# Kernel optimization log

Measured on AMD Instinct MI355X. Metric: run time of the kernel, lower is better.

The kernel has to match this reference:

```python
import jax, jax.numpy as jnp
import numpy as np

N_NODES = 100000
D = 128
ATT = 128
P_EDGE_TYPES = 3
N_EDGES = 1600000
BATCH = 65536


def gcn_conv(x, W, b, src, dst, n):
    # PyG GCNConv: add self loops, symmetric D^{-1/2} (A+I) D^{-1/2} x W + b
    h = x @ W                                   # [N, D]
    ones = jnp.ones(src.shape[0], x.dtype)
    deg = jax.ops.segment_sum(ones, dst, num_segments=n) + 1.0  # +1 self loop
    dinv = jax.lax.rsqrt(deg)
    norm = dinv[src] * dinv[dst]                # [E]
    out = jax.ops.segment_sum(h[src] * norm[:, None], dst, num_segments=n)
    out = out + h * (dinv * dinv)[:, None]      # self-loop message, norm = dinv_i^2
    return out + b


def semantic_attention(z, P, W, b, q):
    # z: [P*N, D] -> per-edge-type scalar attention, softmax over P, weighted sum
    att = jnp.tanh(z @ W + b) @ q               # [P*N]
    att = att.reshape(P, -1).mean(axis=1)       # [P]
    att = jax.nn.softmax(att)
    zp = z.reshape(P, -1, z.shape[-1])          # [P, N, D]
    return jnp.einsum('p,pnd->nd', att, zp)     # [N, D]


def gnn_branch(x0, edge_index, W1, b1, W2, b2, n):
    outs = []
    for t in range(edge_index.shape[0]):        # fixed small set of edge types
        src, dst = edge_index[t, 0], edge_index[t, 1]
        h = jax.nn.relu(gcn_conv(x0, W1, b1, src, dst, n))
        h = jax.nn.relu(gcn_conv(h, W2, b2, src, dst, n))
        outs.append(h)
    return jnp.concatenate(outs, axis=0)        # [P*N, D]


def setup_inputs() -> dict:
    key = jax.random.key(0)
    ks = jax.random.split(key, 16)
    x = jax.random.normal(ks[0], (N_NODES, D), jnp.float32)
    edge_index = jax.random.randint(ks[1], (P_EDGE_TYPES, 2, N_EDGES), 0, N_NODES, jnp.int64)
    perm = jax.random.permutation(ks[2], N_NODES).astype(jnp.int64)
    summary_vetor = jax.random.normal(ks[3], (D,), jnp.float32)
    s = 1.0 / np.sqrt(D)
    params = dict(
        W_lin=jax.random.normal(ks[4], (D, D), jnp.float32) * s,
        b_lin=jnp.zeros((D,), jnp.float32),
        W1=jax.random.normal(ks[5], (D, D), jnp.float32) * s,
        b1=jnp.zeros((D,), jnp.float32),
        W2=jax.random.normal(ks[6], (D, D), jnp.float32) * s,
        b2=jnp.zeros((D,), jnp.float32),
        W_sem=jax.random.normal(ks[7], (D, ATT), jnp.float32) * s,
        b_sem=jnp.zeros((ATT,), jnp.float32),
        q_sem=jax.random.normal(ks[8], (ATT,), jnp.float32) * (1.0 / np.sqrt(ATT)),
        W_disc=jax.random.normal(ks[9], (D, D), jnp.float32) * s,
        b_disc=jnp.zeros((), jnp.float32),
    )
    return dict(x=x, edge_index=edge_index, perm=perm,
                summary_vetor=summary_vetor, Batch_size=BATCH, **params)


def reference(x, edge_index, perm, summary_vetor, Batch_size,
              W_lin, b_lin, W1, b1, W2, b2, W_sem, b_sem, q_sem, W_disc, b_disc):
    n = x.shape[0]
    x_pos = jax.nn.relu(x @ W_lin + b_lin)
    x_neg = jax.nn.relu(x[perm] @ W_lin + b_lin)

    z_pos = gnn_branch(x_pos, edge_index, W1, b1, W2, b2, n)
    z_neg = gnn_branch(x_neg, edge_index, W1, b1, W2, b2, n)

    P = edge_index.shape[0]
    att_pos = semantic_attention(z_pos, P, W_sem, b_sem, q_sem)[:Batch_size]
    att_neg = semantic_attention(z_neg, P, W_sem, b_sem, q_sem)[:Batch_size]

    summary_in = att_pos.mean(axis=0)           # AvgReadout
    summary = 0.5 * (summary_vetor + summary_in)

    # Discriminator: bilinear score against broadcast summary
    c = W_disc @ summary                        # [D]
    sc_pos = att_pos @ c + b_disc               # [B]
    sc_neg = att_neg @ c + b_disc               # [B]
    ret = jnp.concatenate([sc_pos, sc_neg], axis=0)  # [2B]
    return ret, summary
```

## Files before the change

kernel.cpp:

```cpp
#include <hip/hip_runtime.h>

#define D_ 128
#define BATCH_ 65536
#define BSH 10
#define TILE_ 16384

typedef _Float16 f16;
typedef _Float16 h2v __attribute__((ext_vector_type(2)));
typedef _Float16 f16x8 __attribute__((ext_vector_type(8)));
typedef float f32x4 __attribute__((ext_vector_type(4)));

__global__ void k_zero32(uint32_t* p, long long n) {
    long long i = (long long)blockIdx.x * blockDim.x + threadIdx.x;
    long long st = (long long)gridDim.x * blockDim.x;
    for (; i < n; i += st) p[i] = 0u;
}

__global__ void k_sentinel(float* p, long long n) {
    long long i = (long long)blockIdx.x * blockDim.x + threadIdx.x;
    long long st = (long long)gridDim.x * blockDim.x;
    for (; i < n; i += st) p[i] = -12345.0f;
}

__global__ void k_wt(const float* __restrict__ W, f16* __restrict__ Wt) {
    int t = blockIdx.x * 256 + threadIdx.x;
    int k = t >> 7, c = t & 127;
    Wt[c * 128 + k] = (f16)W[k * 128 + c];
}

__global__ void k_gath(const uint32_t* __restrict__ src, const int* __restrict__ perm,
                       uint32_t* __restrict__ dst, int N) {
    int i = blockIdx.x * 256 + threadIdx.x;
    if (i >= N * 64) return;
    int row = i >> 6, col = i & 63;
    dst[i] = src[((size_t)perm[row] << 6) + col];
}

__global__ void k_hist(const int* __restrict__ ei, int* __restrict__ bcnt,
                       int E, int nbt, int nbuk) {
    __shared__ int hist[512];
    for (int i = threadIdx.x; i < 512; i += 256) hist[i] = 0;
    __syncthreads();
    long long tot = 3LL * E;
    long long i = (long long)blockIdx.x * 256 + threadIdx.x;
    long long st = (long long)gridDim.x * 256;
    for (; i < tot; i += st) {
        int t = (i >= E) + (i >= 2LL * E);
        long long w = i - (long long)t * E;
        int dst = ei[(long long)t * 2 * E + E + w];
        atomicAdd(&hist[t * nbt + (dst >> BSH)], 1);
    }
    __syncthreads();
    for (int i2 = threadIdx.x; i2 < nbuk; i2 += 256)
        if (hist[i2]) atomicAdd(&bcnt[i2], hist[i2]);
}

__global__ void k_bscan(const int* __restrict__ bcnt, int* __restrict__ bbase,
                        int* __restrict__ bcur, int nbuk) {
    __shared__ int s[512];
    int t = threadIdx.x;
    int v = (t < nbuk) ? bcnt[t] : 0;
    s[t] = v;
    __syncthreads();
    for (int off = 1; off < 512; off <<= 1) {
        int a = (t >= off) ? s[t - off] : 0;
        __syncthreads();
        s[t] += a;
        __syncthreads();
    }
    if (t < nbuk) {
        int e = s[t] - v;
        bbase[t] = e;
        bcur[t] = e;
        if (t == nbuk - 1) bbase[nbuk] = s[t];
    }
}

__global__ __launch_bounds__(256) void k_scatter(const int* __restrict__ ei,
                                                 int* __restrict__ bcur,
                                                 uint32_t* __restrict__ pairs,
                                                 int E, int nbt, int nbuk) {
    __shared__ int hist[512];
    __shared__ int base[512];
    long long tot = 3LL * E;
    long long w0 = (long long)blockIdx.x * TILE_;
    long long w1 = w0 + TILE_ < tot ? w0 + TILE_ : tot;
    for (int i = threadIdx.x; i < 512; i += 256) hist[i] = 0;
    __syncthreads();
    for (long long e = w0 + threadIdx.x; e < w1; e += 256) {
        int t = (e >= E) + (e >= 2LL * E);
        long long w = e - (long long)t * E;
        int dst = ei[(long long)t * 2 * E + E + w];
        atomicAdd(&hist[t * nbt + (dst >> BSH)], 1);
    }
    __syncthreads();
    for (int i = threadIdx.x; i < nbuk; i += 256) {
        int c = hist[i];
        base[i] = c ? atomicAdd(&bcur[i], c) : 0;
        hist[i] = 0;
    }
    __syncthreads();
    for (long long e = w0 + threadIdx.x; e < w1; e += 256) {
        int t = (e >= E) + (e >= 2LL * E);
        long long w = e - (long long)t * E;
        int src = ei[(long long)t * 2 * E + w];
        int dst = ei[(long long)t * 2 * E + E + w];
        int b = t * nbt + (dst >> BSH);
        int off = atomicAdd(&hist[b], 1);
        pairs[base[b] + off] = (uint32_t)src | ((uint32_t)(dst & ((1 << BSH) - 1)) << 22);
    }
}

__global__ __launch_bounds__(256) void k_bucket(const uint32_t* __restrict__ pairs,
                                                const int* __restrict__ bbase,
                                                int* __restrict__ rowstart,
                                                float* __restrict__ dinv,
                                                int* __restrict__ csr,
                                                int N, int nbt, int nbuk, int L) {
    __shared__ int cnt[1024];
    __shared__ int pref[1024];
    __shared__ int sums[256];
    int b = blockIdx.x;
    int t = b / nbt, bb = b - t * nbt;
    int dst0 = bb << BSH;
    int ndst = (N - dst0 < 1024) ? (N - dst0) : 1024;
    int e0 = bbase[b], e1 = bbase[b + 1];
    int tid = threadIdx.x;
    for (int i = tid; i < 1024; i += 256) cnt[i] = 0;
    __syncthreads();
    for (int e = e0 + tid; e < e1; e += 256) atomicAdd(&cnt[pairs[e] >> 22], 1);
    __syncthreads();
    int i0 = tid * 4;
    int c0 = cnt[i0], c1 = cnt[i0 + 1], c2 = cnt[i0 + 2], c3 = cnt[i0 + 3];
    int s4 = c0 + c1 + c2 + c3;
    sums[tid] = s4;
    __syncthreads();
    for (int off = 1; off < 256; off <<= 1) {
        int v = (tid >= off) ? sums[tid - off] : 0;
        __syncthreads();
        sums[tid] += v;
        __syncthreads();
    }
    int run = sums[tid] - s4;
    pref[i0] = run; run += c0;
    pref[i0 + 1] = run; run += c1;
    pref[i0 + 2] = run; run += c2;
    pref[i0 + 3] = run;
    __syncthreads();
    for (int d = tid; d < ndst; d += 256) {
        int r = t * N + dst0 + d;
        rowstart[r] = e0 + pref[d];
        dinv[r] = rsqrtf((float)cnt[d] + 1.0f);
    }
    if (b == nbuk - 1 && tid == 0) rowstart[L] = e1;
    __syncthreads();
    for (int e = e0 + tid; e < e1; e += 256) {
        uint32_t u = pairs[e];
        int d = u >> 22;
        int pos = e0 + atomicAdd(&pref[d], 1);
        csr[pos] = (int)(u & ((1u << 22) - 1));
    }
}

__global__ void k_wedge(const int* __restrict__ csr, const float* __restrict__ dinv,
                        f16* __restrict__ w16, int N, int E) {
    long long tot = 3LL * E;
    long long i = (long long)blockIdx.x * 256 + threadIdx.x;
    long long st = (long long)gridDim.x * 256;
    for (; i < tot; i += st) {
        int t = (i >= E) + (i >= 2LL * E);
        w16[i] = (f16)dinv[t * N + csr[i]];
    }
}

__global__ __launch_bounds__(256) void k_mgemm(const void* __restrict__ in, int in_f32,
                                               const f16* __restrict__ Wt,
                                               const float* __restrict__ bias,
                                               f16* __restrict__ outh, int n, int relu) {
    int l = threadIdx.x & 63, wid = threadIdx.x >> 6;
    int row0 = blockIdx.x * 128 + wid * 32;
    int r = l & 15, kg = l >> 4;
    f32x4 acc[2][8] = {};
#pragma unroll
    for (int kk = 0; kk < 4; kk++) {
        int off = kk * 32 + kg * 8;
        f16x8 a[2];
#pragma unroll
        for (int h = 0; h < 2; h++) {
            int arow = row0 + h * 16 + r;
            f16x8 av = {};
            if (arow < n) {
                if (in_f32) {
                    const float* inf = (const float*)in + (size_t)arow * D_ + off;
                    float4 v0 = *(const float4*)inf;
                    float4 v1 = *(const float4*)(inf + 4);
                    av[0] = (f16)v0.x; av[1] = (f16)v0.y; av[2] = (f16)v0.z; av[3] = (f16)v0.w;
                    av[4] = (f16)v1.x; av[5] = (f16)v1.y; av[6] = (f16)v1.z; av[7] = (f16)v1.w;
                } else {
                    av = *(const f16x8*)((const f16*)in + (size_t)arow * D_ + off);
                }
            }
            a[h] = av;
        }
#pragma unroll
        for (int ct = 0; ct < 8; ct++) {
            f16x8 b = *(const f16x8*)(Wt + (size_t)(ct * 16 + r) * D_ + off);
            acc[0][ct] = __builtin_amdgcn_mfma_f32_16x16x32_f16(a[0], b, acc[0][ct], 0, 0, 0);
            acc[1][ct] = __builtin_amdgcn_mfma_f32_16x16x32_f16(a[1], b, acc[1][ct], 0, 0, 0);
        }
    }
#pragma unroll
    for (int h = 0; h < 2; h++) {
#pragma unroll
        for (int ct = 0; ct < 8; ct++) {
            int c = ct * 16 + r;
            float bs = bias ? bias[c] : 0.0f;
#pragma unroll
            for (int j = 0; j < 4; j++) {
                int rr = row0 + h * 16 + kg * 4 + j;
                if (rr >= n) continue;
                float o = acc[h][ct][j] + bs;
                if (relu) o = fmaxf(o, 0.0f);
                outh[(size_t)rr * D_ + c] = (f16)o;
            }
        }
    }
}

__global__ __launch_bounds__(256) void k_spmm1g(const f16* __restrict__ gsrc,
                                                const int* __restrict__ csr,
                                                const f16* __restrict__ w16,
                                                const int* __restrict__ rowstart,
                                                const float* __restrict__ dinv,
                                                const float* __restrict__ bias,
                                                const f16* __restrict__ Wt,
                                                f16* __restrict__ outG,
                                                int N, int rows, int src_typed) {
    __shared__ f16 hs[16][136];
    int tid = (int)threadIdx.x;
    int lp = tid & 15;
    int row16 = tid >> 4;
    int gw0 = blockIdx.x * 16;
    int gw = gw0 + row16;
    bool valid = gw < rows;
    float a[8] = {};
    if (valid) {
        int t = (gw >= N) + (gw >= 2 * N);
        int tbase = t * N;
        int sbase = src_typed ? tbase : 0;
        int self = src_typed ? gw : gw - tbase;
        int s0 = rowstart[gw], s1 = rowstart[gw + 1];
        float di = dinv[gw];
        size_t co = (size_t)(lp << 3);
        const f16* gp = gsrc + co;
        {
            f16x8 sv = *(const f16x8*)(gp + (size_t)self * D_);
#pragma unroll
            for (int u = 0; u < 8; u++) a[u] = (float)sv[u] * di;
        }
        int j = s0;
        for (; j + 2 <= s1; j += 2) {
            int sA = csr[j], sB = csr[j + 1];
            float wA = (float)w16[j], wB = (float)w16[j + 1];
            f16x8 vA = *(const f16x8*)(gp + (size_t)(sbase + sA) * D_);
            f16x8 vB = *(const f16x8*)(gp + (size_t)(sbase + sB) * D_);
#pragma unroll
            for (int u = 0; u < 8; u++) a[u] = fmaf((float)vA[u], wA, a[u]);
#pragma unroll
            for (int u = 0; u < 8; u++) a[u] = fmaf((float)vB[u], wB, a[u]);
        }
        if (j < s1) {
            int s = csr[j];
            float w = (float)w16[j];
            f16x8 v = *(const f16x8*)(gp + (size_t)(sbase + s) * D_);
#pragma unroll
            for (int u = 0; u < 8; u++) a[u] = fmaf((float)v[u], w, a[u]);
        }
        float4 b0 = *(const float4*)(bias + co);
        float4 b1v = *(const float4*)(bias + co + 4);
        a[0] = fmaxf(fmaf(a[0], di, b0.x), 0.f);
        a[1] = fmaxf(fmaf(a[1], di, b0.y), 0.f);
        a[2] = fmaxf(fmaf(a[2], di, b0.z), 0.f);
        a[3] = fmaxf(fmaf(a[3], di, b0.w), 0.f);
        a[4] = fmaxf(fmaf(a[4], di, b1v.x), 0.f);
        a[5] = fmaxf(fmaf(a[5], di, b1v.y), 0.f);
        a[6] = fmaxf(fmaf(a[6], di, b1v.z), 0.f);
        a[7] = fmaxf(fmaf(a[7], di, b1v.w), 0.f);
    }
    f16x8 hv;
#pragma unroll
    for (int u = 0; u < 8; u++) hv[u] = (f16)a[u];
    *(f16x8*)&hs[row16][lp << 3] = hv;
    __syncthreads();
    int l = tid & 63, wid = tid >> 6;
    int r = l & 15, kg = l >> 4;
    f16x8 af[4];
#pragma unroll
    for (int kk = 0; kk < 4; kk++) af[kk] = *(const f16x8*)&hs[r][kk * 32 + kg * 8];
#pragma unroll
    for (int ct = 0; ct < 2; ct++) {
        int c = wid * 32 + ct * 16 + r;
        f32x4 acc = {};
#pragma unroll
        for (int kk = 0; kk < 4; kk++) {
            f16x8 b = *(const f16x8*)(Wt + (size_t)c * D_ + kk * 32 + kg * 8);
            acc = __builtin_amdgcn_mfma_f32_16x16x32_f16(af[kk], b, acc, 0, 0, 0);
        }
#pragma unroll
        for (int j = 0; j < 4; j++) {
            int rr = gw0 + kg * 4 + j;
            if (rr < rows) outG[(size_t)rr * D_ + c] = (f16)acc[j];
        }
    }
}

__global__ __launch_bounds__(256) void k_spmm2a(const f16* __restrict__ gsrc,
                                                const int* __restrict__ csr,
                                                const f16* __restrict__ w16,
                                                const int* __restrict__ rowstart,
                                                const float* __restrict__ dinv,
                                                const float* __restrict__ bias,
                                                const f16* __restrict__ Wst,
                                                const float* __restrict__ bsem,
                                                const float* __restrict__ q,
                                                f16* __restrict__ outZ,
                                                float* __restrict__ att_part,
                                                int N, int rows, int src_typed) {
    __shared__ f16 hs[16][136];
    __shared__ float ws[4];
    int tid = (int)threadIdx.x;
    int lp = tid & 15;
    int row16 = tid >> 4;
    int gw0 = blockIdx.x * 16;
    int gw = gw0 + row16;
    bool valid = gw < rows;
    float a[8] = {};
    if (valid) {
        int t = (gw >= N) + (gw >= 2 * N);
        int tbase = t * N;
        int sbase = src_typed ? tbase : 0;
        int self = src_typed ? gw : gw - tbase;
        int s0 = rowstart[gw], s1 = rowstart[gw + 1];
        float di = dinv[gw];
        size_t co = (size_t)(lp << 3);
        const f16* gp = gsrc + co;
        {
            f16x8 sv = *(const f16x8*)(gp + (size_t)self * D_);
#pragma unroll
            for (int u = 0; u < 8; u++) a[u] = (float)sv[u] * di;
        }
        int j = s0;
        for (; j + 2 <= s1; j += 2) {
            int sA = csr[j], sB = csr[j + 1];
            float wA = (float)w16[j], wB = (float)w16[j + 1];
            f16x8 vA = *(const f16x8*)(gp + (size_t)(sbase + sA) * D_);
            f16x8 vB = *(const f16x8*)(gp + (size_t)(sbase + sB) * D_);
#pragma unroll
            for (int u = 0; u < 8; u++) a[u] = fmaf((float)vA[u], wA, a[u]);
#pragma unroll
            for (int u = 0; u < 8; u++) a[u] = fmaf((float)vB[u], wB, a[u]);
        }
        if (j < s1) {
            int s = csr[j];
            float w = (float)w16[j];
            f16x8 v = *(const f16x8*)(gp + (size_t)(sbase + s) * D_);
#pragma unroll
            for (int u = 0; u < 8; u++) a[u] = fmaf((float)v[u], w, a[u]);
        }
        float4 b0 = *(const float4*)(bias + co);
        float4 b1v = *(const float4*)(bias + co + 4);
        a[0] = fmaxf(fmaf(a[0], di, b0.x), 0.f);
        a[1] = fmaxf(fmaf(a[1], di, b0.y), 0.f);
        a[2] = fmaxf(fmaf(a[2], di, b0.z), 0.f);
        a[3] = fmaxf(fmaf(a[3], di, b0.w), 0.f);
        a[4] = fmaxf(fmaf(a[4], di, b1v.x), 0.f);
        a[5] = fmaxf(fmaf(a[5], di, b1v.y), 0.f);
        a[6] = fmaxf(fmaf(a[6], di, b1v.z), 0.f);
        a[7] = fmaxf(fmaf(a[7], di, b1v.w), 0.f);
    }
    f16x8 hv;
#pragma unroll
    for (int u = 0; u < 8; u++) hv[u] = (f16)a[u];
    *(f16x8*)&hs[row16][lp << 3] = hv;
    if (valid) *(f16x8*)(outZ + (size_t)gw * D_ + (size_t)(lp << 3)) = hv;
    __syncthreads();
    int l = tid & 63, wid = tid >> 6;
    int r = l & 15, kg = l >> 4;
    f16x8 af[4];
#pragma unroll
    for (int kk = 0; kk < 4; kk++) af[kk] = *(const f16x8*)&hs[r][kk * 32 + kg * 8];
    float s = 0.0f;
#pragma unroll
    for (int ct = 0; ct < 2; ct++) {
        int c = wid * 32 + ct * 16 + r;
        f32x4 acc = {};
#pragma unroll
        for (int kk = 0; kk < 4; kk++) {
            f16x8 b = *(const f16x8*)(Wst + (size_t)c * D_ + kk * 32 + kg * 8);
            acc = __builtin_amdgcn_mfma_f32_16x16x32_f16(af[kk], b, acc, 0, 0, 0);
        }
        float qc = q[c], bc = bsem[c];
#pragma unroll
        for (int j = 0; j < 4; j++) {
            int rr = gw0 + kg * 4 + j;
            if (rr < rows) s += qc * tanhf(acc[j] + bc);
        }
    }
#pragma unroll
    for (int m = 1; m < 64; m <<= 1) s += __shfl_xor(s, m, 64);
    if (l == 0) ws[wid] = s;
    __syncthreads();
    if (tid == 0) {
        int t = (gw0 >= N) + (gw0 >= 2 * N);
        atomicAdd(&att_part[((blockIdx.x & 63) << 2) + t], ws[0] + ws[1] + ws[2] + ws[3]);
    }
}

__global__ void k_attw(const float* __restrict__ att_part, float* __restrict__ att_w, float invN) {
    __shared__ float sb[3];
    int t = threadIdx.x;
    if (t < 3) {
        float s = 0.f;
        for (int i = 0; i < 64; i++) s += att_part[(i << 2) + t];
        sb[t] = s * invN;
    }
    __syncthreads();
    if (t == 0) {
        float m = fmaxf(sb[0], fmaxf(sb[1], sb[2]));
        float x0 = expf(sb[0] - m), x1 = expf(sb[1] - m), x2 = expf(sb[2] - m);
        float inv = 1.f / (x0 + x1 + x2);
        att_w[0] = x0 * inv; att_w[1] = x1 * inv; att_w[2] = x2 * inv;
    }
}

__global__ __launch_bounds__(256) void k_colsum(const f16* __restrict__ Z, size_t tstride,
                                                const float* __restrict__ att_w,
                                                float* __restrict__ colsum) {
    int c2 = threadIdx.x & 63;
    int rg = threadIdx.x >> 6;
    int nbase = blockIdx.x << 7;
    float w0 = att_w[0], w1 = att_w[1], w2 = att_w[2];
    float csx = 0.f, csy = 0.f;
    for (int i = rg; i < 128; i += 4) {
        size_t off = (size_t)(nbase + i) * D_ + (c2 << 1);
        h2v z0 = *(const h2v*)(Z + off);
        h2v z1 = *(const h2v*)(Z + tstride + off);
        h2v z2 = *(const h2v*)(Z + 2 * tstride + off);
        csx += w0 * (float)z0.x + w1 * (float)z1.x + w2 * (float)z2.x;
        csy += w0 * (float)z0.y + w1 * (float)z1.y + w2 * (float)z2.y;
    }
    __shared__ float red[4][128];
    red[rg][c2 << 1] = csx;
    red[rg][(c2 << 1) + 1] = csy;
    __syncthreads();
    if (rg == 0) {
        float sx = red[0][c2 << 1] + red[1][c2 << 1] + red[2][c2 << 1] + red[3][c2 << 1];
        float sy = red[0][(c2 << 1) + 1] + red[1][(c2 << 1) + 1] + red[2][(c2 << 1) + 1] + red[3][(c2 << 1) + 1];
        atomicAdd(&colsum[c2 << 1], sx);
        atomicAdd(&colsum[(c2 << 1) + 1], sy);
    }
}

__global__ void k_summary_c(const float* __restrict__ colsum, const float* __restrict__ sv,
                            const float* __restrict__ Wd, float* __restrict__ cvec,
                            float* __restrict__ out_summary) {
    __shared__ float sl[128];
    int t = threadIdx.x;
    float s = 0.5f * (sv[t] + colsum[t] * (1.0f / (float)BATCH_));
    sl[t] = s;
    out_summary[t] = s;
    __syncthreads();
    float a = 0.f;
    for (int j = 0; j < 128; j++) a = fmaf(Wd[t * D_ + j], sl[j], a);
    cvec[t] = a;
}

__global__ __launch_bounds__(256) void k_cscore(const f16* __restrict__ Z, size_t tstride,
                                                const float* __restrict__ att_w,
                                                const float* __restrict__ c,
                                                const float* __restrict__ bd,
                                                float* __restrict__ out, int B) {
    int gw = (int)((blockIdx.x * (long long)blockDim.x + threadIdx.x) >> 6);
    int lane = threadIdx.x & 63;
    if (gw >= B) return;
    size_t off = (size_t)gw * D_ + (lane << 1);
    float w0 = att_w[0], w1 = att_w[1], w2 = att_w[2];
    h2v z0 = *(const h2v*)(Z + off);
    h2v z1 = *(const h2v*)(Z + tstride + off);
    h2v z2 = *(const h2v*)(Z + 2 * tstride + off);
    float vx = w0 * (float)z0.x + w1 * (float)z1.x + w2 * (float)z2.x;
    float vy = w0 * (float)z0.y + w1 * (float)z1.y + w2 * (float)z2.y;
    float2 cc = *(const float2*)(c + (lane << 1));
    float a = vx * cc.x + vy * cc.y;
#pragma unroll
    for (int m = 1; m < 64; m <<= 1) a += __shfl_xor(a, m, 64);
    if (lane == 0) out[gw] = a + bd[0];
}

extern "C" void kernel_launch(void* const* d_in, const int* in_sizes, int n_in,
                              void* d_out, int out_size, void* d_ws, size_t ws_size,
                              hipStream_t stream) {
    const float* x      = (const float*)d_in[0];
    const int*   ei     = (const int*)d_in[1];
    const int*   perm   = (const int*)d_in[2];
    const float* sv     = (const float*)d_in[3];
    const float* W_lin  = (const float*)d_in[5];
    const float* b_lin  = (const float*)d_in[6];
    const float* W1     = (const float*)d_in[7];
    const float* b1     = (const float*)d_in[8];
    const float* W2     = (const float*)d_in[9];
    const float* b2     = (const float*)d_in[10];
    const float* W_sem  = (const float*)d_in[11];
    const float* b_sem  = (const float*)d_in[12];
    const float* q_sem  = (const float*)d_in[13];
    const float* W_disc = (const float*)d_in[14];
    const float* b_disc = (const float*)d_in[15];
    float* out = (float*)d_out;

    int N = in_sizes[0] / D_;
    int E = in_sizes[1] / 6;
    int L = 3 * N;
    size_t ND = (size_t)N * D_;
    int B = BATCH_;
    int nbt = (N + (1 << BSH) - 1) >> BSH;
    int nbuk = 3 * nbt;

    char* ws = (char*)d_ws;
    size_t o = 0;
    auto alloc = [&](size_t bytes) -> char* {
        char* p = ws + o;
        o = (o + bytes + 255) & ~(size_t)255;
        return p;
    };
    float* dinv     = (float*)alloc((size_t)L * 4);
    int*   rowstart = (int*)alloc(((size_t)L + 1) * 4);
    int*   csr      = (int*)alloc(((size_t)3 * E + 16) * 4);
    int*   bcnt     = (int*)alloc(512 * 4);
    int*   bbase    = (int*)alloc(513 * 4);
    int*   bcur     = (int*)alloc(512 * 4);
    float* att_part = (float*)alloc(256 * 4);
    float* att_w    = (float*)alloc(16 * 4);
    float* colsum   = (float*)alloc(128 * 4);
    float* cvec     = (float*)alloc(128 * 4);
    f16*   Wlt      = (f16*)alloc(128 * 128 * 2);
    f16*   W1t      = (f16*)alloc(128 * 128 * 2);
    f16*   W2t      = (f16*)alloc(128 * 128 * 2);
    f16*   Wst      = (f16*)alloc(128 * 128 * 2);
    f16*   Ah       = (f16*)alloc(ND * 2);
    f16*   G1h      = (f16*)alloc(ND * 2);
    f16*   G1p      = (f16*)alloc(ND * 2);
    f16*   G2all    = (f16*)alloc(3 * ND * 2);
    f16*   Zall     = (f16*)alloc(3 * ND * 2);
    size_t o_full = o;

    uint32_t* pairs = (uint32_t*)Zall;
    f16*      w16  = (f16*)Ah;

    if (o_full > ws_size || N >= (1 << 22) || (N & 15) || nbuk > 512 ||
        (size_t)3 * E * 4 > 3 * ND * 2 || (size_t)3 * E * 2 > ND * 2) {
        k_sentinel<<<256, 256, 0, stream>>>(out, out_size);
        return;
    }

    k_wt<<<64, 256, 0, stream>>>(W_lin, Wlt);
    k_wt<<<64, 256, 0, stream>>>(W1, W1t);
    k_wt<<<64, 256, 0, stream>>>(W2, W2t);
    k_wt<<<64, 256, 0, stream>>>(W_sem, Wst);

    long long tot = 3LL * E;
    k_zero32<<<2, 256, 0, stream>>>((uint32_t*)bcnt, 512);
    k_hist<<<2048, 256, 0, stream>>>(ei, bcnt, E, nbt, nbuk);
    k_bscan<<<1, 512, 0, stream>>>(bcnt, bbase, bcur, nbuk);
    int scat_grid = (int)((tot + TILE_ - 1) / TILE_);
    k_scatter<<<scat_grid, 256, 0, stream>>>(ei, bcur, pairs, E, nbt, nbuk);
    k_bucket<<<nbuk, 256, 0, stream>>>(pairs, bbase, rowstart, dinv, csr, N, nbt, nbuk, L);

    int mgN_grid  = (N + 127) / 128;
    int spmm_grid = (L + 15) / 16;
    int scoreB_grid = (B + 3) / 4;

    k_mgemm<<<mgN_grid, 256, 0, stream>>>(x, 1, Wlt, b_lin, Ah, N, 1);
    k_mgemm<<<mgN_grid, 256, 0, stream>>>(Ah, 0, W1t, nullptr, G1h, N, 0);
    k_gath<<<(N * 64 + 255) / 256, 256, 0, stream>>>((const uint32_t*)G1h, perm,
                                                     (uint32_t*)G1p, N);
    k_wedge<<<2048, 256, 0, stream>>>(csr, dinv, w16, N, E);

    for (int br = 0; br < 2; br++) {
        const f16* src1 = br ? G1p : G1h;
        float* aw = att_w + br * 8;
        k_zero32<<<1, 256, 0, stream>>>((uint32_t*)att_part, 256);
        k_spmm1g<<<spmm_grid, 256, 0, stream>>>(src1, csr, w16, rowstart, dinv, b1,
                                                W2t, G2all, N, L, 0);
        k_spmm2a<<<spmm_grid, 256, 0, stream>>>(G2all, csr, w16, rowstart, dinv, b2,
                                                Wst, b_sem, q_sem, Zall, att_part, N, L, 1);
        k_attw<<<1, 64, 0, stream>>>(att_part, aw, 1.0f / (float)N);
        if (br == 0) {
            k_zero32<<<1, 256, 0, stream>>>((uint32_t*)colsum, 128);
            k_colsum<<<512, 256, 0, stream>>>(Zall, ND, aw, colsum);
            k_summary_c<<<1, 128, 0, stream>>>(colsum, sv, W_disc, cvec, out + 2 * (size_t)B);
            k_cscore<<<scoreB_grid, 256, 0, stream>>>(Zall, ND, aw, cvec, b_disc, out, B);
        } else {
            k_cscore<<<scoreB_grid, 256, 0, stream>>>(Zall, ND, aw, cvec, b_disc, out + B, B);
        }
    }
}
```

Baseline: 1.248 ms.

## Sort rows by degree within each edge type for balanced SpMM blocks

Adds a counting sort of destination rows by in-degree (capped at 255) within each edge type, and makes both SpMM kernels process rows in that order, scattering outputs through the row index. Rows in the same wavefront then have similar neighbor-loop lengths, which reduces divergence and tail imbalance. The second-layer output is now stored only for the first B rows of each type, shrinking the Z buffer and the readout traffic. The cost is extra preprocessing kernels and scattered, less coalesced output writes. It also relies on N being a multiple of 16 and each block holding rows of a single edge type.

```diff
diff --git a/kernel.cpp b/kernel.cpp
--- a/kernel.cpp
+++ b/kernel.cpp
@@ -162,6 +162,42 @@
     }
 }
 
+__global__ void k_dhist(const int* __restrict__ rowstart, int* __restrict__ dh,
+                        int N, int L) {
+    int r = blockIdx.x * 256 + threadIdx.x;
+    if (r >= L) return;
+    int deg = rowstart[r + 1] - rowstart[r];
+    if (deg > 255) deg = 255;
+    int t = (r >= N) + (r >= 2 * N);
+    atomicAdd(&dh[t * 256 + deg], 1);
+}
+
+__global__ void k_dscan(const int* __restrict__ dh, int* __restrict__ dcur, int nb) {
+    __shared__ int s[1024];
+    int t = threadIdx.x;
+    int v = (t < nb) ? dh[t] : 0;
+    s[t] = v;
+    __syncthreads();
+    for (int off = 1; off < 1024; off <<= 1) {
+        int a = (t >= off) ? s[t - off] : 0;
+        __syncthreads();
+        s[t] += a;
+        __syncthreads();
+    }
+    if (t < nb) dcur[t] = s[t] - v;
+}
+
+__global__ void k_dorder(const int* __restrict__ rowstart, int* __restrict__ dcur,
+                         int* __restrict__ ord, int N, int L) {
+    int r = blockIdx.x * 256 + threadIdx.x;
+    if (r >= L) return;
+    int deg = rowstart[r + 1] - rowstart[r];
+    if (deg > 255) deg = 255;
+    int t = (r >= N) + (r >= 2 * N);
+    int pos = atomicAdd(&dcur[t * 256 + deg], 1);
+    ord[pos] = r;
+}
+
 __global__ void k_wedge(const int* __restrict__ csr, const float* __restrict__ dinv,
                         f16* __restrict__ w16, int N, int E) {
     long long tot = 3LL * E;
@@ -234,59 +270,57 @@
                                                 const float* __restrict__ dinv,
                                                 const float* __restrict__ bias,
                                                 const f16* __restrict__ Wt,
+                                                const int* __restrict__ ord,
                                                 f16* __restrict__ outG,
-                                                int N, int rows, int src_typed) {
+                                                int N, int rows) {
     __shared__ f16 hs[16][136];
+    __shared__ int rid[16];
     int tid = (int)threadIdx.x;
     int lp = tid & 15;
     int row16 = tid >> 4;
-    int gw0 = blockIdx.x * 16;
-    int gw = gw0 + row16;
-    bool valid = gw < rows;
-    float a[8] = {};
-    if (valid) {
-        int t = (gw >= N) + (gw >= 2 * N);
-        int tbase = t * N;
-        int sbase = src_typed ? tbase : 0;
-        int self = src_typed ? gw : gw - tbase;
-        int s0 = rowstart[gw], s1 = rowstart[gw + 1];
-        float di = dinv[gw];
-        size_t co = (size_t)(lp << 3);
-        const f16* gp = gsrc + co;
-        {
-            f16x8 sv = *(const f16x8*)(gp + (size_t)self * D_);
-#pragma unroll
-            for (int u = 0; u < 8; u++) a[u] = (float)sv[u] * di;
-        }
-        int j = s0;
-        for (; j + 2 <= s1; j += 2) {
-            int sA = csr[j], sB = csr[j + 1];
-            float wA = (float)w16[j], wB = (float)w16[j + 1];
-            f16x8 vA = *(const f16x8*)(gp + (size_t)(sbase + sA) * D_);
-            f16x8 vB = *(const f16x8*)(gp + (size_t)(sbase + sB) * D_);
-#pragma unroll
-            for (int u = 0; u < 8; u++) a[u] = fmaf((float)vA[u], wA, a[u]);
-#pragma unroll
-            for (int u = 0; u < 8; u++) a[u] = fmaf((float)vB[u], wB, a[u]);
-        }
-        if (j < s1) {
-            int s = csr[j];
-            float w = (float)w16[j];
-            f16x8 v = *(const f16x8*)(gp + (size_t)(sbase + s) * D_);
-#pragma unroll
-            for (int u = 0; u < 8; u++) a[u] = fmaf((float)v[u], w, a[u]);
-        }
-        float4 b0 = *(const float4*)(bias + co);
-        float4 b1v = *(const float4*)(bias + co + 4);
-        a[0] = fmaxf(fmaf(a[0], di, b0.x), 0.f);
-        a[1] = fmaxf(fmaf(a[1], di, b0.y), 0.f);
-        a[2] = fmaxf(fmaf(a[2], di, b0.z), 0.f);
-        a[3] = fmaxf(fmaf(a[3], di, b0.w), 0.f);
-        a[4] = fmaxf(fmaf(a[4], di, b1v.x), 0.f);
-        a[5] = fmaxf(fmaf(a[5], di, b1v.y), 0.f);
-        a[6] = fmaxf(fmaf(a[6], di, b1v.z), 0.f);
-        a[7] = fmaxf(fmaf(a[7], di, b1v.w), 0.f);
-    }
+    int gw = ord[blockIdx.x * 16 + row16];
+    if (lp == 0) rid[row16] = gw;
+    int t = (gw >= N) + (gw >= 2 * N);
+    int tbase = t * N;
+    int self = gw - tbase;
+    int s0 = rowstart[gw], s1 = rowstart[gw + 1];
+    float di = dinv[gw];
+    size_t co = (size_t)(lp << 3);
+    const f16* gp = gsrc + co;
+    float a[8];
+    {
+        f16x8 sv = *(const f16x8*)(gp + (size_t)self * D_);
+#pragma unroll
+        for (int u = 0; u < 8; u++) a[u] = (float)sv[u] * di;
+    }
+    int j = s0;
+    for (; j + 2 <= s1; j += 2) {
+        int sA = csr[j], sB = csr[j + 1];
+        float wA = (float)w16[j], wB = (float)w16[j + 1];
+        f16x8 vA = *(const f16x8*)(gp + (size_t)sA * D_);
+        f16x8 vB = *(const f16x8*)(gp + (size_t)sB * D_);
+#pragma unroll
+        for (int u = 0; u < 8; u++) a[u] = fmaf((float)vA[u], wA, a[u]);
+#pragma unroll
+        for (int u = 0; u < 8; u++) a[u] = fmaf((float)vB[u], wB, a[u]);
+    }
+    if (j < s1) {
+        int s = csr[j];
+        float w = (float)w16[j];
+        f16x8 v = *(const f16x8*)(gp + (size_t)s * D_);
+#pragma unroll
+        for (int u = 0; u < 8; u++) a[u] = fmaf((float)v[u], w, a[u]);
+    }
+    float4 b0 = *(const float4*)(bias + co);
+    float4 b1v = *(const float4*)(bias + co + 4);
+    a[0] = fmaxf(fmaf(a[0], di, b0.x), 0.f);
+    a[1] = fmaxf(fmaf(a[1], di, b0.y), 0.f);
+    a[2] = fmaxf(fmaf(a[2], di, b0.z), 0.f);
+    a[3] = fmaxf(fmaf(a[3], di, b0.w), 0.f);
+    a[4] = fmaxf(fmaf(a[4], di, b1v.x), 0.f);
+    a[5] = fmaxf(fmaf(a[5], di, b1v.y), 0.f);
+    a[6] = fmaxf(fmaf(a[6], di, b1v.z), 0.f);
+    a[7] = fmaxf(fmaf(a[7], di, b1v.w), 0.f);
     f16x8 hv;
 #pragma unroll
     for (int u = 0; u < 8; u++) hv[u] = (f16)a[u];
@@ -307,9 +341,9 @@
             acc = __builtin_amdgcn_mfma_f32_16x16x32_f16(af[kk], b, acc, 0, 0, 0);
         }
 #pragma unroll
-        for (int j = 0; j < 4; j++) {
-            int rr = gw0 + kg * 4 + j;
-            if (rr < rows) outG[(size_t)rr * D_ + c] = (f16)acc[j];
+        for (int j2 = 0; j2 < 4; j2++) {
+            int grow = rid[kg * 4 + j2];
+            outG[(size_t)grow * D_ + c] = (f16)acc[j2];
         }
     }
 }
@@ -323,66 +357,65 @@
                                                 const f16* __restrict__ Wst,
                                                 const float* __restrict__ bsem,
                                                 const float* __restrict__ q,
-                                                f16* __restrict__ outZ,
+                                                const int* __restrict__ ord,
+                                                f16* __restrict__ Zb,
                                                 float* __restrict__ att_part,
-                                                int N, int rows, int src_typed) {
+                                                int N, int rows, int B) {
     __shared__ f16 hs[16][136];
     __shared__ float ws[4];
+    __shared__ int stype;
     int tid = (int)threadIdx.x;
     int lp = tid & 15;
     int row16 = tid >> 4;
-    int gw0 = blockIdx.x * 16;
-    int gw = gw0 + row16;
-    bool valid = gw < rows;
-    float a[8] = {};
-    if (valid) {
-        int t = (gw >= N) + (gw >= 2 * N);
-        int tbase = t * N;
-        int sbase = src_typed ? tbase : 0;
-        int self = src_typed ? gw : gw - tbase;
-        int s0 = rowstart[gw], s1 = rowstart[gw + 1];
-        float di = dinv[gw];
-        size_t co = (size_t)(lp << 3);
-        const f16* gp = gsrc + co;
-        {
-            f16x8 sv = *(const f16x8*)(gp + (size_t)self * D_);
-#pragma unroll
-            for (int u = 0; u < 8; u++) a[u] = (float)sv[u] * di;
-        }
-        int j = s0;
-        for (; j + 2 <= s1; j += 2) {
-            int sA = csr[j], sB = csr[j + 1];
-            float wA = (float)w16[j], wB = (float)w16[j + 1];
-            f16x8 vA = *(const f16x8*)(gp + (size_t)(sbase + sA) * D_);
-            f16x8 vB = *(const f16x8*)(gp + (size_t)(sbase + sB) * D_);
-#pragma unroll
-            for (int u = 0; u < 8; u++) a[u] = fmaf((float)vA[u], wA, a[u]);
-#pragma unroll
-            for (int u = 0; u < 8; u++) a[u] = fmaf((float)vB[u], wB, a[u]);
-        }
-        if (j < s1) {
-            int s = csr[j];
-            float w = (float)w16[j];
-            f16x8 v = *(const f16x8*)(gp + (size_t)(sbase + s) * D_);
-#pragma unroll
-            for (int u = 0; u < 8; u++) a[u] = fmaf((float)v[u], w, a[u]);
-        }
-        float4 b0 = *(const float4*)(bias + co);
-        float4 b1v = *(const float4*)(bias + co + 4);
-        a[0] = fmaxf(fmaf(a[0], di, b0.x), 0.f);
-        a[1] = fmaxf(fmaf(a[1], di, b0.y), 0.f);
-        a[2] = fmaxf(fmaf(a[2], di, b0.z), 0.f);
-        a[3] = fmaxf(fmaf(a[3], di, b0.w), 0.f);
-        a[4] = fmaxf(fmaf(a[4], di, b1v.x), 0.f);
-        a[5] = fmaxf(fmaf(a[5], di, b1v.y), 0.f);
-        a[6] = fmaxf(fmaf(a[6], di, b1v.z), 0.f);
-        a[7] = fmaxf(fmaf(a[7], di, b1v.w), 0.f);
-    }
+    int gw = ord[blockIdx.x * 16 + row16];
+    int t = (gw >= N) + (gw >= 2 * N);
+    if (tid == 0) stype = t;
+    int tbase = t * N;
+    int self = gw;
+    int s0 = rowstart[gw], s1 = rowstart[gw + 1];
+    float di = dinv[gw];
+    size_t co = (size_t)(lp << 3);
+    const f16* gp = gsrc + co;
+    float a[8];
+    {
+        f16x8 sv = *(const f16x8*)(gp + (size_t)self * D_);
+#pragma unroll
+        for (int u = 0; u < 8; u++) a[u] = (float)sv[u] * di;
+    }
+    int j = s0;
+    for (; j + 2 <= s1; j += 2) {
+        int sA = tbase + csr[j], sB = tbase + csr[j + 1];
+        float wA = (float)w16[j], wB = (float)w16[j + 1];
+        f16x8 vA = *(const f16x8*)(gp + (size_t)sA * D_);
+        f16x8 vB = *(const f16x8*)(gp + (size_t)sB * D_);
+#pragma unroll
+        for (int u = 0; u < 8; u++) a[u] = fmaf((float)vA[u], wA, a[u]);
+#pragma unroll
+        for (int u = 0; u < 8; u++) a[u] = fmaf((float)vB[u], wB, a[u]);
+    }
+    if (j < s1) {
+        int s = tbase + csr[j];
+        float w = (float)w16[j];
+        f16x8 v = *(const f16x8*)(gp + (size_t)s * D_);
+#pragma unroll
+        for (int u = 0; u < 8; u++) a[u] = fmaf((float)v[u], w, a[u]);
+    }
+    float4 b0 = *(const float4*)(bias + co);
+    float4 b1v = *(const float4*)(bias + co + 4);
+    a[0] = fmaxf(fmaf(a[0], di, b0.x), 0.f);
+    a[1] = fmaxf(fmaf(a[1], di, b0.y), 0.f);
+    a[2] = fmaxf(fmaf(a[2], di, b0.z), 0.f);
+    a[3] = fmaxf(fmaf(a[3], di, b0.w), 0.f);
+    a[4] = fmaxf(fmaf(a[4], di, b1v.x), 0.f);
+    a[5] = fmaxf(fmaf(a[5], di, b1v.y), 0.f);
+    a[6] = fmaxf(fmaf(a[6], di, b1v.z), 0.f);
+    a[7] = fmaxf(fmaf(a[7], di, b1v.w), 0.f);
     f16x8 hv;
 #pragma unroll
     for (int u = 0; u < 8; u++) hv[u] = (f16)a[u];
     *(f16x8*)&hs[row16][lp << 3] = hv;
-    if (valid) *(f16x8*)(outZ + (size_t)gw * D_ + (size_t)(lp << 3)) = hv;
+    int local = gw - tbase;
+    if (local < B) *(f16x8*)(Zb + ((size_t)t * B + local) * D_ + co) = hv;
     __syncthreads();
     int l = tid & 63, wid = tid >> 6;
     int r = l & 15, kg = l >> 4;
@@ -401,19 +434,14 @@
         }
         float qc = q[c], bc = bsem[c];
 #pragma unroll
-        for (int j = 0; j < 4; j++) {
-            int rr = gw0 + kg * 4 + j;
-            if (rr < rows) s += qc * tanhf(acc[j] + bc);
-        }
+        for (int j2 = 0; j2 < 4; j2++) s += qc * tanhf(acc[j2] + bc);
     }
 #pragma unroll
     for (int m = 1; m < 64; m <<= 1) s += __shfl_xor(s, m, 64);
     if (l == 0) ws[wid] = s;
     __syncthreads();
-    if (tid == 0) {
-        int t = (gw0 >= N) + (gw0 >= 2 * N);
-        atomicAdd(&att_part[((blockIdx.x & 63) << 2) + t], ws[0] + ws[1] + ws[2] + ws[3]);
-    }
+    if (tid == 0)
+        atomicAdd(&att_part[((blockIdx.x & 63) << 2) + stype], ws[0] + ws[1] + ws[2] + ws[3]);
 }
 
 __global__ void k_attw(const float* __restrict__ att_part, float* __restrict__ att_w, float invN) {
@@ -522,6 +550,7 @@
     int L = 3 * N;
     size_t ND = (size_t)N * D_;
     int B = BATCH_;
+    size_t BD = (size_t)B * D_;
     int nbt = (N + (1 << BSH) - 1) >> BSH;
     int nbuk = 3 * nbt;
 
@@ -535,9 +564,12 @@
     float* dinv     = (float*)alloc((size_t)L * 4);
     int*   rowstart = (int*)alloc(((size_t)L + 1) * 4);
     int*   csr      = (int*)alloc(((size_t)3 * E + 16) * 4);
+    int*   ord      = (int*)alloc((size_t)L * 4);
     int*   bcnt     = (int*)alloc(512 * 4);
     int*   bbase    = (int*)alloc(513 * 4);
     int*   bcur     = (int*)alloc(512 * 4);
+    int*   dh       = (int*)alloc(768 * 4);
+    int*   dcur     = (int*)alloc(768 * 4);
     float* att_part = (float*)alloc(256 * 4);
     float* att_w    = (float*)alloc(16 * 4);
     float* colsum   = (float*)alloc(128 * 4);
@@ -550,14 +582,14 @@
     f16*   G1h      = (f16*)alloc(ND * 2);
     f16*   G1p      = (f16*)alloc(ND * 2);
     f16*   G2all    = (f16*)alloc(3 * ND * 2);
-    f16*   Zall     = (f16*)alloc(3 * ND * 2);
+    f16*   Zb       = (f16*)alloc(3 * BD * 2);
     size_t o_full = o;
 
-    uint32_t* pairs = (uint32_t*)Zall;
+    uint32_t* pairs = (uint32_t*)Zb;
     f16*      w16  = (f16*)Ah;
 
-    if (o_full > ws_size || N >= (1 << 22) || (N & 15) || nbuk > 512 ||
-        (size_t)3 * E * 4 > 3 * ND * 2 || (size_t)3 * E * 2 > ND * 2) {
+    if (o_full > ws_size || N >= (1 << 22) || (N & 15) || nbuk > 512 || B > N ||
+        (size_t)3 * E * 4 > 3 * BD * 2 || (size_t)3 * E * 2 > ND * 2) {
         k_sentinel<<<256, 256, 0, stream>>>(out, out_size);
         return;
     }
@@ -575,8 +607,13 @@
     k_scatter<<<scat_grid, 256, 0, stream>>>(ei, bcur, pairs, E, nbt, nbuk);
     k_bucket<<<nbuk, 256, 0, stream>>>(pairs, bbase, rowstart, dinv, csr, N, nbt, nbuk, L);
 
+    k_zero32<<<2, 256, 0, stream>>>((uint32_t*)dh, 768);
+    k_dhist<<<(L + 255) / 256, 256, 0, stream>>>(rowstart, dh, N, L);
+    k_dscan<<<1, 1024, 0, stream>>>(dh, dcur, 768);
+    k_dorder<<<(L + 255) / 256, 256, 0, stream>>>(rowstart, dcur, ord, N, L);
+
     int mgN_grid  = (N + 127) / 128;
-    int spmm_grid = (L + 15) / 16;
+    int spmm_grid = L / 16;
     int scoreB_grid = (B + 3) / 4;
 
     k_mgemm<<<mgN_grid, 256, 0, stream>>>(x, 1, Wlt, b_lin, Ah, N, 1);
@@ -590,17 +627,18 @@
         float* aw = att_w + br * 8;
         k_zero32<<<1, 256, 0, stream>>>((uint32_t*)att_part, 256);
         k_spmm1g<<<spmm_grid, 256, 0, stream>>>(src1, csr, w16, rowstart, dinv, b1,
-                                                W2t, G2all, N, L, 0);
+                                                W2t, ord, G2all, N, L);
         k_spmm2a<<<spmm_grid, 256, 0, stream>>>(G2all, csr, w16, rowstart, dinv, b2,
-                                                Wst, b_sem, q_sem, Zall, att_part, N, L, 1);
+                                                Wst, b_sem, q_sem, ord, Zb, att_part,
+                                                N, L, B);
         k_attw<<<1, 64, 0, stream>>>(att_part, aw, 1.0f / (float)N);
         if (br == 0) {
             k_zero32<<<1, 256, 0, stream>>>((uint32_t*)colsum, 128);
-            k_colsum<<<512, 256, 0, stream>>>(Zall, ND, aw, colsum);
+            k_colsum<<<512, 256, 0, stream>>>(Zb, BD, aw, colsum);
             k_summary_c<<<1, 128, 0, stream>>>(colsum, sv, W_disc, cvec, out + 2 * (size_t)B);
-            k_cscore<<<scoreB_grid, 256, 0, stream>>>(Zall, ND, aw, cvec, b_disc, out, B);
+            k_cscore<<<scoreB_grid, 256, 0, stream>>>(Zb, BD, aw, cvec, b_disc, out, B);
         } else {
-            k_cscore<<<scoreB_grid, 256, 0, stream>>>(Zall, ND, aw, cvec, b_disc, out + B, B);
+            k_cscore<<<scoreB_grid, 256, 0, stream>>>(Zb, BD, aw, cvec, b_disc, out + B, B);
         }
     }
 }
```

After: 1.997 ms. 1.6x slower.
